# Kernel tuning notes

Hardware: AMD Instinct MI355X
Metric: run time of the kernel (lower is better)

## Reference

```python
import jax, jax.numpy as jnp
import numpy as np

WS = 7          # window size
NUM_HEADS = 8


def _depthwise_conv3x3(x, w, b):
    # x: [B, C, H, W], w: [C, 1, 3, 3], groups=C depthwise, padding=1
    y = jax.lax.conv_general_dilated(
        x, w, window_strides=(1, 1), padding='SAME',
        dimension_numbers=('NCHW', 'OIHW', 'NCHW'),
        feature_group_count=x.shape[1])
    return y + b[None, :, None, None]


def setup_inputs() -> dict:
    key = jax.random.key(0)
    k1, k2, k3 = jax.random.split(key, 3)
    B, H, W, C = 8, 112, 112, 256
    qkv = jax.random.normal(k1, (3, B, H * W, C), dtype=jnp.float32)
    lepe_w = jax.random.normal(k2, (C, 1, 3, 3), dtype=jnp.float32) * 0.1
    lepe_b = jax.random.normal(k3, (C,), dtype=jnp.float32) * 0.1
    return {"qkv": qkv, "lepe_w": lepe_w, "lepe_b": lepe_b, "H": H, "W": W}


def reference(qkv, lepe_w, lepe_b, H, W):
    q, k, v = qkv[0], qkv[1], qkv[2]          # each [B, N, C]
    B, N, C = v.shape
    hd = C // NUM_HEADS
    scale = hd ** -0.5
    Gh, Gw = H // WS, W // WS                 # H, W assumed divisible by WS

    # LePE: depthwise 3x3 conv on v viewed as image
    lepe = _depthwise_conv3x3(v.transpose(0, 2, 1).reshape(B, C, H, W), lepe_w, lepe_b)
    lepe = lepe.reshape(B, C, N).transpose(0, 2, 1)   # [B, N, C]

    def to_windows(x):
        # [B, N, C] -> [B*Gh*Gw, heads, ws*ws, hd]
        x = x.reshape(B, Gh, WS, Gw, WS, NUM_HEADS, hd)
        return x.transpose(0, 1, 3, 5, 2, 4, 6).reshape(B * Gh * Gw, NUM_HEADS, WS * WS, hd)

    qg = to_windows(q) * scale
    kg = to_windows(k)
    vg = to_windows(v)

    attn = jax.nn.softmax(jnp.einsum('ghnd,ghmd->ghnm', qg, kg), axis=-1)
    out = jnp.einsum('ghnm,ghmd->ghnd', attn, vg)     # [BG, heads, n, hd]

    # group2image: inverse window partition -> [B, N, C]
    out = out.reshape(B, Gh, Gw, NUM_HEADS, WS, WS, hd)
    out = out.transpose(0, 1, 4, 2, 5, 3, 6).reshape(B, N, C)
    return out + lepe
```

## Files before the change

### kernel.cpp

```cpp
#include <hip/hip_runtime.h>

#define WS   7
#define NH   8
#define HD   32
#define WIN  49
#define HALO 9
#define VHST 36
#define PST  72
#define LST  34

typedef __fp16 h2  __attribute__((ext_vector_type(2)));
typedef __fp16 v4h __attribute__((ext_vector_type(4)));
typedef float  v4f __attribute__((ext_vector_type(4)));

__global__ __launch_bounds__(64)
void win_attn_lepe(const float* __restrict__ qkv,
                   const float* __restrict__ lw,
                   const float* __restrict__ lb,
                   float* __restrict__ out,
                   int B, int H, int W, int C)
{
    const int N  = H * W;
    const int Gw = W / WS;
    const int G  = (H / WS) * Gw;

    const int unit = blockIdx.x;
    const int wid  = unit >> 3;
    const int h    = unit & 7;
    const int b    = wid / G;
    const int g    = wid % G;
    const int gy   = g / Gw, gx = g % Gw;
    const int row0 = gy * WS, col0 = gx * WS;
    const int c0   = h * HD;

    const size_t plane = (size_t)B * N * C;
    const float* qb = qkv + (size_t)b * N * C;
    const float* kb = qb + plane;
    const float* vb = qb + 2 * plane;

    const int l  = threadIdx.x;
    const int lr = l & 15;
    const int gq = l >> 4;

    __shared__ __fp16 sVh  [HALO * HALO * VHST];
    __shared__ __fp16 sW2  [16 * 20];
    __shared__ __fp16 sLepe[WIN * LST];
    __shared__ __fp16 sP   [16 * PST];

    for (int idx = l; idx < HALO * HALO * 8; idx += 64) {
        int p  = idx >> 3;
        int d4 = (idx & 7) * 4;
        int ry = row0 - 1 + p / HALO, rx = col0 - 1 + p % HALO;
        bool in = (ry >= 0 && ry < H && rx >= 0 && rx < W);
        float4 f = make_float4(0.f, 0.f, 0.f, 0.f);
        if (in) f = *reinterpret_cast<const float4*>(vb + ((size_t)ry * W + rx) * C + c0 + d4);
        h2 a  = __builtin_amdgcn_cvt_pkrtz(f.x, f.y);
        h2 b2 = __builtin_amdgcn_cvt_pkrtz(f.z, f.w);
        v4h v4 = { a.x, a.y, b2.x, b2.y };
        *reinterpret_cast<v4h*>(&sVh[p * VHST + d4]) = v4;
    }
    for (int i = l; i < 288; i += 64) {
        int d = i / 9, t = i - d * 9;
        sW2[(d >> 1) * 20 + 2 * t + (d & 1)] = (__fp16)lw[(size_t)(c0 + d) * 9 + t];
    }
    __syncthreads();

    const float bias0 = lb[c0 + lr];
    const float bias1 = lb[c0 + 16 + lr];

    auto pixoff = [&](int p) -> size_t {
        p = p > 48 ? 48 : p;
        int r = row0 + p / WS, c = col0 + p % WS;
        return ((size_t)r * W + c) * C + c0;
    };

    const float scale = 0.17677669529663687f;

    v4h qf[4][2];
    #pragma unroll
    for (int m = 0; m < 4; ++m) {
        size_t off = pixoff(16 * m + lr);
        #pragma unroll
        for (int s = 0; s < 2; ++s) {
            float4 f = *reinterpret_cast<const float4*>(qb + off + 16 * s + 4 * gq);
            h2 a  = __builtin_amdgcn_cvt_pkrtz(f.x * scale, f.y * scale);
            h2 b2 = __builtin_amdgcn_cvt_pkrtz(f.z * scale, f.w * scale);
            qf[m][s] = v4h{ a.x, a.y, b2.x, b2.y };
        }
    }
    v4h kf[4][2];
    #pragma unroll
    for (int t = 0; t < 4; ++t) {
        size_t off = pixoff(16 * t + lr);
        #pragma unroll
        for (int s = 0; s < 2; ++s) {
            float4 f = *reinterpret_cast<const float4*>(kb + off + 16 * s + 4 * gq);
            h2 a  = __builtin_amdgcn_cvt_pkrtz(f.x, f.y);
            h2 b2 = __builtin_amdgcn_cvt_pkrtz(f.z, f.w);
            kf[t][s] = v4h{ a.x, a.y, b2.x, b2.y };
        }
    }

    v4h vf[4][2];
    #pragma unroll
    for (int s4 = 0; s4 < 4; ++s4) {
        #pragma unroll
        for (int j = 0; j < 4; ++j) {
            int p  = 16 * s4 + 4 * gq + j;
            int pc = p > 48 ? 48 : p;
            int hp = (pc / WS + 1) * HALO + pc % WS + 1;
            int base = hp * VHST + lr;
            vf[s4][0][j] = sVh[base];
            vf[s4][1][j] = sVh[base + 16];
        }
    }

    {
        h2 w2r[9];
        #pragma unroll
        for (int t = 0; t < 9; ++t)
            w2r[t] = *reinterpret_cast<const h2*>(&sW2[lr * 20 + 2 * t]);
        #pragma unroll 1
        for (int it = 0; it < 13; ++it) {
            int pix = it * 4 + gq;
            if (pix < WIN) {
                int wy = pix / WS, wx = pix - (pix / WS) * WS;
                h2 acc = h2{ (__fp16)0.f, (__fp16)0.f };
                #pragma unroll
                for (int dh = 0; dh < 3; ++dh)
                    #pragma unroll
                    for (int dw = 0; dw < 3; ++dw) {
                        h2 v = *reinterpret_cast<const h2*>(
                            &sVh[((wy + dh) * HALO + (wx + dw)) * VHST + 2 * lr]);
                        acc += w2r[dh * 3 + dw] * v;
                    }
                *reinterpret_cast<h2*>(&sLepe[pix * LST + 2 * lr]) = acc;
            }
        }
    }
    __syncthreads();

    const v4h ones = { (__fp16)1.f, (__fp16)1.f, (__fp16)1.f, (__fp16)1.f };

    #pragma unroll 1
    for (int m = 0; m < 4; ++m) {
        v4f sa[4] = { v4f{0,0,0,0}, v4f{0,0,0,0}, v4f{0,0,0,0}, v4f{0,0,0,0} };
        #pragma unroll
        for (int t = 0; t < 4; ++t)
            #pragma unroll
            for (int s = 0; s < 2; ++s)
                sa[t] = __builtin_amdgcn_mfma_f32_16x16x16f16(qf[m][s], kf[t][s], sa[t], 0, 0, 0);

        #pragma unroll
        for (int t = 0; t < 4; ++t) {
            bool valid = (16 * t + lr) < WIN;
            #pragma unroll
            for (int r = 0; r < 4; ++r) {
                float e = valid ? __expf(sa[t][r] - 3.f) : 0.f;
                sP[(4 * gq + r) * PST + 16 * t + lr] = (__fp16)e;
            }
        }
        __syncthreads();

        v4f oa0 = v4f{0,0,0,0}, oa1 = v4f{0,0,0,0}, od = v4f{0,0,0,0};
        #pragma unroll
        for (int s4 = 0; s4 < 4; ++s4) {
            v4h pa = *reinterpret_cast<const v4h*>(&sP[lr * PST + 16 * s4 + 4 * gq]);
            oa0 = __builtin_amdgcn_mfma_f32_16x16x16f16(pa, vf[s4][0], oa0, 0, 0, 0);
            oa1 = __builtin_amdgcn_mfma_f32_16x16x16f16(pa, vf[s4][1], oa1, 0, 0, 0);
            od  = __builtin_amdgcn_mfma_f32_16x16x16f16(pa, ones,      od,  0, 0, 0);
        }
        __syncthreads();

        #pragma unroll
        for (int r = 0; r < 4; ++r) {
            int p = 16 * m + 4 * gq + r;
            if (p < WIN) {
                float inv = __builtin_amdgcn_rcpf(od[r]);
                int rr = row0 + p / WS, cc = col0 + p % WS;
                float* dst = out + ((size_t)b * N + (size_t)rr * W + cc) * C + c0 + lr;
                dst[0]  = oa0[r] * inv + (float)sLepe[p * LST + lr]      + bias0;
                dst[16] = oa1[r] * inv + (float)sLepe[p * LST + 16 + lr] + bias1;
            }
        }
    }
}

extern "C" void kernel_launch(void* const* d_in, const int* in_sizes, int n_in,
                              void* d_out, int out_size, void* d_ws, size_t ws_size,
                              hipStream_t stream) {
    const float* qkv = (const float*)d_in[0];
    const float* lw  = (const float*)d_in[1];
    const float* lb  = (const float*)d_in[2];
    float* out = (float*)d_out;

    const int H = 112, W = 112;
    const int C = in_sizes[2];
    const int N = H * W;
    const int B = in_sizes[0] / (3 * N * C);
    const int G = (H / WS) * (W / WS);

    const int units = B * G * NH;
    win_attn_lepe<<<units, 64, 0, stream>>>(qkv, lw, lb, out, B, H, W, C);
}
```

Before: 148.0 us.

## Keep softmax probabilities in registers via transposed QK MFMA layout

```diff
diff --git a/kernel.cpp b/kernel.cpp
--- a/kernel.cpp
+++ b/kernel.cpp
@@ -6,7 +6,6 @@
 #define WIN  49
 #define HALO 9
 #define VHST 36
-#define PST  72
 #define LST  34
 
 typedef __fp16 h2  __attribute__((ext_vector_type(2)));
@@ -45,7 +44,6 @@
     __shared__ __fp16 sVh  [HALO * HALO * VHST];
     __shared__ __fp16 sW2  [16 * 20];
     __shared__ __fp16 sLepe[WIN * LST];
-    __shared__ __fp16 sP   [16 * PST];
 
     for (int idx = l; idx < HALO * HALO * 8; idx += 64) {
         int p  = idx >> 3;
@@ -140,47 +138,46 @@
     }
     __syncthreads();
 
-    const v4h ones = { (__fp16)1.f, (__fp16)1.f, (__fp16)1.f, (__fp16)1.f };
-
     #pragma unroll 1
-    for (int m = 0; m < 4; ++m) {
+    for (int mq = 0; mq < 4; ++mq) {
         v4f sa[4] = { v4f{0,0,0,0}, v4f{0,0,0,0}, v4f{0,0,0,0}, v4f{0,0,0,0} };
         #pragma unroll
-        for (int t = 0; t < 4; ++t)
+        for (int tk = 0; tk < 4; ++tk)
             #pragma unroll
             for (int s = 0; s < 2; ++s)
-                sa[t] = __builtin_amdgcn_mfma_f32_16x16x16f16(qf[m][s], kf[t][s], sa[t], 0, 0, 0);
-
-        #pragma unroll
-        for (int t = 0; t < 4; ++t) {
-            bool valid = (16 * t + lr) < WIN;
+                sa[tk] = __builtin_amdgcn_mfma_f32_16x16x16f16(kf[tk][s], qf[mq][s], sa[tk], 0, 0, 0);
+
+        float den = 0.f;
+        #pragma unroll
+        for (int tk = 0; tk < 4; ++tk)
             #pragma unroll
             for (int r = 0; r < 4; ++r) {
-                float e = valid ? __expf(sa[t][r] - 3.f) : 0.f;
-                sP[(4 * gq + r) * PST + 16 * t + lr] = (__fp16)e;
+                float e = (16 * tk + 4 * gq + r < WIN) ? __expf(sa[tk][r] - 3.f) : 0.f;
+                sa[tk][r] = e;
+                den += e;
             }
-        }
-        __syncthreads();
-
-        v4f oa0 = v4f{0,0,0,0}, oa1 = v4f{0,0,0,0}, od = v4f{0,0,0,0};
+        den += __shfl_xor(den, 16);
+        den += __shfl_xor(den, 32);
+        const float inv = __builtin_amdgcn_rcpf(den);
+
+        v4f oa0 = v4f{0,0,0,0}, oa1 = v4f{0,0,0,0};
         #pragma unroll
         for (int s4 = 0; s4 < 4; ++s4) {
-            v4h pa = *reinterpret_cast<const v4h*>(&sP[lr * PST + 16 * s4 + 4 * gq]);
+            h2 p01 = __builtin_amdgcn_cvt_pkrtz(sa[s4][0] * inv, sa[s4][1] * inv);
+            h2 p23 = __builtin_amdgcn_cvt_pkrtz(sa[s4][2] * inv, sa[s4][3] * inv);
+            v4h pa = v4h{ p01.x, p01.y, p23.x, p23.y };
             oa0 = __builtin_amdgcn_mfma_f32_16x16x16f16(pa, vf[s4][0], oa0, 0, 0, 0);
             oa1 = __builtin_amdgcn_mfma_f32_16x16x16f16(pa, vf[s4][1], oa1, 0, 0, 0);
-            od  = __builtin_amdgcn_mfma_f32_16x16x16f16(pa, ones,      od,  0, 0, 0);
-        }
-        __syncthreads();
+        }
 
         #pragma unroll
         for (int r = 0; r < 4; ++r) {
-            int p = 16 * m + 4 * gq + r;
+            int p = 16 * mq + 4 * gq + r;
             if (p < WIN) {
-                float inv = __builtin_amdgcn_rcpf(od[r]);
                 int rr = row0 + p / WS, cc = col0 + p % WS;
                 float* dst = out + ((size_t)b * N + (size_t)rr * W + cc) * C + c0 + lr;
-                dst[0]  = oa0[r] * inv + (float)sLepe[p * LST + lr]      + bias0;
-                dst[16] = oa1[r] * inv + (float)sLepe[p * LST + 16 + lr] + bias1;
+                dst[0]  = oa0[r] + (float)sLepe[p * LST + lr]      + bias0;
+                dst[16] = oa1[r] + (float)sLepe[p * LST + 16 + lr] + bias1;
             }
         }
     }
```

Result: no change. 145.8 us (-1.5%).
